# Performance work log

Hardware: AMD Instinct MI355X
Metric: run time of the kernel (lower is better)

## Reference

```python
import jax, jax.numpy as jnp
import numpy as np

NEG_ATT = 0.2   # GATv2Conv internal leaky_relu slope
NEG_ACT = 0.01  # nn.LeakyReLU default slope (activation between layers)

def _segment_softmax(logits, seg, n):
    m = jax.ops.segment_max(logits, seg, num_segments=n)
    ex = jnp.exp(logits - m[seg])
    s = jax.ops.segment_sum(ex, seg, num_segments=n)
    return ex / s[seg]

def _gatv2(h, Wl, bl, Wr, br, att, bias, src, dst, n):
    # PyG GATv2Conv, heads=1: xl = lin_l(h) (source/message), xr = lin_r(h) (target)
    xl = h @ Wl + bl                                   # [N, H]
    xr = h @ Wr + br                                   # [N, H]
    e = jax.nn.leaky_relu(xl[src] + xr[dst], NEG_ATT)  # [E, H]
    logits = e @ att                                   # [E]
    alpha = _segment_softmax(logits, dst, n)           # softmax over incoming edges per dst
    out = jax.ops.segment_sum(xl[src] * alpha[:, None], dst, num_segments=n)
    return out + bias

def setup_inputs() -> dict:
    key = jax.random.key(0)
    G, P, DEG, DIN, H, EX, OUT, NC = 4096, 24, 8, 32, 128, 8, 3, 6
    N = G * P
    E = N * DEG
    ks = jax.random.split(key, 16)
    x = jax.random.normal(ks[0], (N, DIN), jnp.float32)
    gid = jnp.arange(E) // (P * DEG)  # edges stay within their graph
    src = gid * P + jax.random.randint(ks[1], (E,), 0, P)
    dst = gid * P + jax.random.randint(ks[2], (E,), 0, P)
    batch = jnp.repeat(jnp.arange(G), P)
    extra_feat = jax.random.normal(ks[3], (G, EX), jnp.float32)
    sc = lambda k, shp: jax.random.normal(k, shp, jnp.float32) * 0.05
    return dict(
        x=x, src=src, dst=dst, batch=batch, extra_feat=extra_feat,
        W_init0=sc(ks[4], (DIN, H)), b_init0=jnp.zeros((H,), jnp.float32),
        W_init1=sc(ks[5], (H, H)), b_init1=jnp.zeros((H,), jnp.float32),
        Wl=sc(ks[6], (NC, H, H)), bl=jnp.zeros((NC, H), jnp.float32),
        Wr=sc(ks[7], (NC, H, H)), br=jnp.zeros((NC, H), jnp.float32),
        att=sc(ks[8], (NC, H)), cbias=jnp.zeros((NC, H), jnp.float32),
        Wf0=sc(ks[9], (H + EX, H)), bf0=jnp.zeros((H,), jnp.float32),
        Wf1=sc(ks[10], (H, H)), bf1=jnp.zeros((H,), jnp.float32),
        Wf2=sc(ks[11], (H, OUT)), bf2=jnp.zeros((OUT,), jnp.float32),
    )

def reference(x, src, dst, batch, extra_feat,
              W_init0, b_init0, W_init1, b_init1,
              Wl, bl, Wr, br, att, cbias,
              Wf0, bf0, Wf1, bf1, Wf2, bf2):
    N = x.shape[0]
    G = extra_feat.shape[0]
    # init MLP
    h = jax.nn.leaky_relu(x @ W_init0 + b_init0, NEG_ACT)
    h = jax.nn.leaky_relu(h @ W_init1 + b_init1, NEG_ACT)
    # GATv2Conv adds self-loops
    loop = jnp.arange(N)
    src_sl = jnp.concatenate([src, loop])
    dst_sl = jnp.concatenate([dst, loop])
    NUM_GAT, MP = 2, 3
    for g in range(NUM_GAT):
        for m in range(MP):
            c = g * MP + m
            h = _gatv2(h, Wl[c], bl[c], Wr[c], br[c], att[c], cbias[c], src_sl, dst_sl, N)
            if m < MP - 1:  # BasicGNN: act between convs, not after last
                h = jax.nn.leaky_relu(h, NEG_ACT)
    # global_add_pool + extra features + final MLP
    pooled = jax.ops.segment_sum(h, batch, num_segments=G)
    z = jnp.concatenate([pooled, extra_feat], axis=1)
    z = jax.nn.leaky_relu(z @ Wf0 + bf0, NEG_ACT)
    z = jax.nn.leaky_relu(z @ Wf1 + bf1, NEG_ACT)
    return z @ Wf2 + bf2
```

## Files before the change

### kernel.cpp

```cpp
#include <hip/hip_runtime.h>

#define NG   4096
#define P    24
#define EPG  192
#define ESL  216
#define DIN  32
#define H    128
#define EX   8
#define NOUT 3
#define HSS  136
#define XTS  36

typedef _Float16 f16x8 __attribute__((ext_vector_type(8)));
typedef _Float16 h2    __attribute__((ext_vector_type(2)));
typedef float    f32x4 __attribute__((ext_vector_type(4)));

__device__ __forceinline__ unsigned short f2h(float v) {
    _Float16 h = (_Float16)v; unsigned short u; __builtin_memcpy(&u, &h, 2); return u;
}
__device__ __forceinline__ float h2f(unsigned short u) {
    _Float16 h; __builtin_memcpy(&h, &u, 2); return (float)h;
}
__device__ __forceinline__ unsigned pkadd(unsigned a, unsigned b) {
    h2 x, y; __builtin_memcpy(&x, &a, 4); __builtin_memcpy(&y, &b, 4);
    h2 z = x + y; unsigned r; __builtin_memcpy(&r, &z, 4); return r;
}
__device__ __forceinline__ float lrelu(float v, float s) { return v > 0.f ? v : v * s; }

__global__ void cvtw(const float* __restrict__ W0, const float* __restrict__ W1,
                     const float* __restrict__ Wl, const float* __restrict__ Wr,
                     const float* __restrict__ att, const float* __restrict__ bl,
                     const float* __restrict__ br, unsigned short* __restrict__ ws) {
    int i = blockIdx.x * 256 + threadIdx.x;
    if (i < 217088) {
        float v;
        if (i < 4096)        { int n = i >> 5, k = i & 31;  v = W0[k * 128 + n]; }
        else if (i < 20480)  { int j = i - 4096;  int n = j >> 7, k = j & 127; v = W1[k * 128 + n]; }
        else if (i < 118784) { int j = i - 20480; int c = j >> 14, r = j & 16383;
                               int n = r >> 7, k = r & 127; v = Wl[c * 16384 + k * 128 + n]; }
        else                 { int j = i - 118784; int c = j >> 14, r = j & 16383;
                               int n = r >> 7, k = r & 127; v = Wr[c * 16384 + k * 128 + n]; }
        ws[i] = f2h(v);
    } else if (i < 241664) {
        int j = i - 217088;
        const float* W = (j < 12288) ? Wl : Wr;
        if (j >= 12288) j -= 12288;
        int c = j >> 11, r = j & 2047, row = r >> 7, k = r & 127;
        float v = 0.f;
        if (row == 0) {
            for (int q = 0; q < 128; ++q) v += W[c * 16384 + k * 128 + q] * att[c * 128 + q];
        }
        ws[i] = f2h(v);
    } else if (i < 241676) {
        int c = i - 241664;
        const float* B = (c < 6) ? bl : br;
        int cc = (c < 6) ? c : c - 6;
        float s = 0.f;
        for (int q = 0; q < 128; ++q) s += B[cc * 128 + q] * att[cc * 128 + q];
        ((float*)(ws + 241664))[c] = s;
    }
}

__global__ __launch_bounds__(256, 4) void gat_all(
    const float* __restrict__ x,
    const int*   __restrict__ src,
    const int*   __restrict__ dst,
    const float* __restrict__ extra,
    const float* __restrict__ b0,  const float* __restrict__ b1,
    const float* __restrict__ bl,  const float* __restrict__ br,
    const float* __restrict__ att, const float* __restrict__ cbias,
    const float* __restrict__ Wf0, const float* __restrict__ bf0,
    const float* __restrict__ Wf1, const float* __restrict__ bf1,
    const float* __restrict__ Wf2, const float* __restrict__ bf2,
    const unsigned short* __restrict__ wsb,
    float* __restrict__ out)
{
    __shared__ __align__(16) unsigned short hb [32 * HSS];
    __shared__ __align__(16) unsigned short xlb[32 * HSS];
    __shared__ __align__(16) unsigned short xrb[32 * HSS];
    __shared__ __align__(16) unsigned short xlT[128 * XTS];
    __shared__ __align__(16) float          Am[1024];
    __shared__ __align__(16) unsigned int   att_h[64];
    __shared__ float dsum[32];
    __shared__ float snode[64];

    const int g    = blockIdx.x;
    const int t    = threadIdx.x;
    const int lane = t & 63;
    const int w    = t >> 6;
    const int m16  = lane & 15;
    const int kc   = lane >> 4;
    const long long gn = (long long)g * P;

    const unsigned short* W0T = wsb;
    const unsigned short* W1T = wsb + 4096;
    const unsigned short* WLT = wsb + 20480;
    const unsigned short* WRT = wsb + 118784;
    const float* wsf = (const float*)(wsb + 241664);

    int s_e = 0, d_e = 0;
    if (t < ESL) {
        if (t < EPG) {
            s_e = src[(long long)g * EPG + t] - (int)gn;
            d_e = dst[(long long)g * EPG + t] - (int)gn;
        } else { s_e = d_e = t - EPG; }
    }

    if (t < 192) {
        float4 v = *reinterpret_cast<const float4*>(&x[gn * DIN + t * 4]);
        int n = t >> 3, k = (t & 7) * 4;
        *reinterpret_cast<ushort4*>(&xlT[n * XTS + k]) =
            make_ushort4(f2h(v.x), f2h(v.y), f2h(v.z), f2h(v.w));
    } else {
        int u = t - 192;
        int r = 24 + (u >> 3), k = (u & 7) * 4;
        *reinterpret_cast<ushort4*>(&xlT[r * XTS + k]) = make_ushort4(0, 0, 0, 0);
    }
    __syncthreads();

    {
        f32x4 acc[4] = {};
        f16x8 a = *reinterpret_cast<const f16x8*>(&xlT[((w & 1) * 16 + m16) * XTS + kc * 8]);
        #pragma unroll
        for (int i = 0; i < 4; ++i) {
            int nt = (w >> 1) * 4 + i;
            f16x8 b = *reinterpret_cast<const f16x8*>(&W0T[(nt * 16 + m16) * 32 + kc * 8]);
            acc[i] = __builtin_amdgcn_mfma_f32_16x16x32_f16(a, b, acc[i], 0, 0, 0);
        }
        #pragma unroll
        for (int i = 0; i < 4; ++i) {
            int col = (w >> 1) * 64 + i * 16 + m16;
            float bv = b0[col];
            #pragma unroll
            for (int r = 0; r < 4; ++r) {
                int row = (w & 1) * 16 + kc * 4 + r;
                xlb[row * HSS + col] = f2h(lrelu(acc[i][r] + bv, 0.01f));
            }
        }
    }
    __syncthreads();

    {
        f32x4 acc[4] = {};
        for (int kt = 0; kt < 4; ++kt) {
            f16x8 a = *reinterpret_cast<const f16x8*>(&xlb[((w & 1) * 16 + m16) * HSS + kt * 32 + kc * 8]);
            #pragma unroll
            for (int i = 0; i < 4; ++i) {
                int nt = (w >> 1) * 4 + i;
                f16x8 b = *reinterpret_cast<const f16x8*>(&W1T[(nt * 16 + m16) * 128 + kt * 32 + kc * 8]);
                acc[i] = __builtin_amdgcn_mfma_f32_16x16x32_f16(a, b, acc[i], 0, 0, 0);
            }
        }
        #pragma unroll
        for (int i = 0; i < 4; ++i) {
            int col = (w >> 1) * 64 + i * 16 + m16;
            float bv = b1[col];
            #pragma unroll
            for (int r = 0; r < 4; ++r) {
                int row = (w & 1) * 16 + kc * 4 + r;
                hb[row * HSS + col] = f2h(lrelu(acc[i][r] + bv, 0.01f));
            }
        }
    }
    __syncthreads();

    for (int c = 0; c < 6; ++c) {
        *reinterpret_cast<float4*>(&Am[t * 4]) = make_float4(0.f, 0.f, 0.f, 0.f);
        if (t < 32) dsum[t] = (t < P) ? 0.f : 1.0f;
        if (t < 64) att_h[t] = ((unsigned)f2h(att[c * H + 2 * t])) |
                               (((unsigned)f2h(att[c * H + 2 * t + 1])) << 16);

        const unsigned short* WT   = ((w & 1) ? WRT : WLT) + c * 16384;
        const unsigned short* WAX  = wsb + 217088 + ((w & 1) ? 12288 : 0) + c * 2048;
        const float*          bias = ((w & 1) ? br : bl) + c * H;
        f32x4 acc[8] = {};
        f32x4 acce[2] = {};
        for (int kt = 0; kt < 4; ++kt) {
            f16x8 a0 = *reinterpret_cast<const f16x8*>(&hb[(m16)      * HSS + kt * 32 + kc * 8]);
            f16x8 a1 = *reinterpret_cast<const f16x8*>(&hb[(16 + m16) * HSS + kt * 32 + kc * 8]);
            #pragma unroll
            for (int i = 0; i < 4; ++i) {
                int nt = (w >> 1) * 4 + i;
                f16x8 b = *reinterpret_cast<const f16x8*>(&WT[(nt * 16 + m16) * 128 + kt * 32 + kc * 8]);
                acc[i]     = __builtin_amdgcn_mfma_f32_16x16x32_f16(a0, b, acc[i],     0, 0, 0);
                acc[4 + i] = __builtin_amdgcn_mfma_f32_16x16x32_f16(a1, b, acc[4 + i], 0, 0, 0);
            }
            if (w >= 2) {
                f16x8 bx = *reinterpret_cast<const f16x8*>(&WAX[m16 * 128 + kt * 32 + kc * 8]);
                acce[0] = __builtin_amdgcn_mfma_f32_16x16x32_f16(a0, bx, acce[0], 0, 0, 0);
                acce[1] = __builtin_amdgcn_mfma_f32_16x16x32_f16(a1, bx, acce[1], 0, 0, 0);
            }
        }
        {
            unsigned short* XO = (w & 1) ? xrb : xlb;
            const bool isL = !(w & 1);
            #pragma unroll
            for (int mt = 0; mt < 2; ++mt)
            #pragma unroll
            for (int i = 0; i < 4; ++i) {
                int col = (w >> 1) * 64 + i * 16 + m16;
                float bv = bias[col];
                unsigned short ub[4];
                #pragma unroll
                for (int r = 0; r < 4; ++r) {
                    int row = mt * 16 + kc * 4 + r;
                    ub[r] = f2h(acc[mt * 4 + i][r] + bv);
                    XO[row * HSS + col] = ub[r];
                }
                if (isL)
                    *reinterpret_cast<ushort4*>(&xlT[col * XTS + mt * 16 + kc * 4]) =
                        make_ushort4(ub[0], ub[1], ub[2], ub[3]);
            }
            if (w >= 2 && m16 == 0) {
                float cst = (w == 2) ? wsf[c] : wsf[6 + c];
                float* dp = (w == 2) ? snode : (snode + 32);
                #pragma unroll
                for (int mt = 0; mt < 2; ++mt)
                #pragma unroll
                for (int r = 0; r < 4; ++r)
                    dp[mt * 16 + kc * 4 + r] = acce[mt][r] + cst;
            }
        }
        __syncthreads();

        if (t < ESL) {
            const uint4* xa = reinterpret_cast<const uint4*>(&xlb[s_e * HSS]);
            const uint4* xb = reinterpret_cast<const uint4*>(&xrb[d_e * HSS]);
            const uint4* ap = reinterpret_cast<const uint4*>(att_h);
            float a0 = 0.f, a1 = 0.f, a2 = 0.f, a3 = 0.f;
            #pragma unroll 4
            for (int cc = 0; cc < 16; ++cc) {
                uint4 wa = xa[cc], wb = xb[cc], pp = ap[cc];
                unsigned u0 = pkadd(wa.x, wb.x) & 0x7fff7fffu;
                unsigned u1 = pkadd(wa.y, wb.y) & 0x7fff7fffu;
                unsigned u2 = pkadd(wa.z, wb.z) & 0x7fff7fffu;
                unsigned u3 = pkadd(wa.w, wb.w) & 0x7fff7fffu;
                asm volatile("v_dot2_f32_f16 %0, %1, %2, %0" : "+v"(a0) : "v"(u0), "v"(pp.x));
                asm volatile("v_dot2_f32_f16 %0, %1, %2, %0" : "+v"(a1) : "v"(u1), "v"(pp.y));
                asm volatile("v_dot2_f32_f16 %0, %1, %2, %0" : "+v"(a2) : "v"(u2), "v"(pp.z));
                asm volatile("v_dot2_f32_f16 %0, %1, %2, %0" : "+v"(a3) : "v"(u3), "v"(pp.w));
            }
            float abss = (a0 + a1) + (a2 + a3);
            float lg = fmaf(0.6f, snode[s_e] + snode[32 + d_e], 0.4f * abss);
            float ex = __expf(lg);
            atomicAdd(&Am[d_e * 32 + s_e], ex);
            atomicAdd(&dsum[d_e], ex);
        }
        __syncthreads();

        {
            int arow = (w & 1) * 16 + m16;
            float4 u0 = *reinterpret_cast<const float4*>(&Am[arow * 32 + kc * 8]);
            float4 u1 = *reinterpret_cast<const float4*>(&Am[arow * 32 + kc * 8 + 4]);
            f16x8 a;
            a[0] = (_Float16)u0.x; a[1] = (_Float16)u0.y;
            a[2] = (_Float16)u0.z; a[3] = (_Float16)u0.w;
            a[4] = (_Float16)u1.x; a[5] = (_Float16)u1.y;
            a[6] = (_Float16)u1.z; a[7] = (_Float16)u1.w;
            f32x4 acc2[4] = {};
            #pragma unroll
            for (int i = 0; i < 4; ++i) {
                int nt = (w >> 1) * 4 + i;
                f16x8 b = *reinterpret_cast<const f16x8*>(&xlT[(nt * 16 + m16) * XTS + kc * 8]);
                acc2[i] = __builtin_amdgcn_mfma_f32_16x16x32_f16(a, b, acc2[i], 0, 0, 0);
            }
            float inv[4];
            #pragma unroll
            for (int r = 0; r < 4; ++r)
                inv[r] = __builtin_amdgcn_rcpf(dsum[(w & 1) * 16 + kc * 4 + r]);
            const bool doact = (c % 3) < 2;
            #pragma unroll
            for (int i = 0; i < 4; ++i) {
                int col = (w >> 1) * 64 + i * 16 + m16;
                float cb = cbias[c * H + col];
                #pragma unroll
                for (int r = 0; r < 4; ++r) {
                    int row = (w & 1) * 16 + kc * 4 + r;
                    float v = fmaf(acc2[i][r], inv[r], cb);
                    if (doact) v = lrelu(v, 0.01f);
                    hb[row * HSS + col] = f2h(v);
                }
            }
        }
        __syncthreads();
    }

    float* z  = Am;
    float* pa = Am + 144;
    float* pb = Am + 288;
    float* h1 = Am + 432;
    float* qa = Am + 576;
    float* qb = Am + 720;
    float* h2 = Am + 864;
    if (t < H) {
        float s = 0.f;
        for (int r = 0; r < P; ++r) s += h2f(hb[r * HSS + t]);
        z[t] = s;
    } else if (t < H + EX) {
        z[t] = extra[(long long)g * EX + (t - H)];
    }
    __syncthreads();
    {
        int j = t & 127, half = t >> 7;
        float a = half ? 0.f : bf0[j];
        int k0 = half ? 68 : 0, k1 = half ? 136 : 68;
        for (int k = k0; k < k1; ++k) a += z[k] * Wf0[k * H + j];
        (half ? pb : pa)[j] = a;
    }
    __syncthreads();
    if (t < H) h1[t] = lrelu(pa[t] + pb[t], 0.01f);
    __syncthreads();
    {
        int j = t & 127, half = t >> 7;
        float a = half ? 0.f : bf1[j];
        int k0 = half * 64, k1 = k0 + 64;
        for (int k = k0; k < k1; ++k) a += h1[k] * Wf1[k * H + j];
        (half ? qb : qa)[j] = a;
    }
    __syncthreads();
    if (t < H) h2[t] = lrelu(qa[t] + qb[t], 0.01f);
    __syncthreads();
    if (t < NOUT) {
        float a = bf2[t];
        for (int k = 0; k < H; ++k) a += h2[k] * Wf2[k * NOUT + t];
        out[(long long)g * NOUT + t] = a;
    }
}

extern "C" void kernel_launch(void* const* d_in, const int* in_sizes, int n_in,
                              void* d_out, int out_size, void* d_ws, size_t ws_size,
                              hipStream_t stream) {
    (void)in_sizes; (void)n_in; (void)out_size; (void)ws_size;
    const float* x     = (const float*)d_in[0];
    const int*   src   = (const int*)  d_in[1];
    const int*   dst   = (const int*)  d_in[2];
    const float* extra = (const float*)d_in[4];
    const float* W0    = (const float*)d_in[5];
    const float* b0    = (const float*)d_in[6];
    const float* W1    = (const float*)d_in[7];
    const float* b1    = (const float*)d_in[8];
    const float* Wl    = (const float*)d_in[9];
    const float* bl    = (const float*)d_in[10];
    const float* Wr    = (const float*)d_in[11];
    const float* br    = (const float*)d_in[12];
    const float* att   = (const float*)d_in[13];
    const float* cbias = (const float*)d_in[14];
    const float* Wf0   = (const float*)d_in[15];
    const float* bf0   = (const float*)d_in[16];
    const float* Wf1   = (const float*)d_in[17];
    const float* bf1   = (const float*)d_in[18];
    const float* Wf2   = (const float*)d_in[19];
    const float* bf2   = (const float*)d_in[20];
    unsigned short* wsb = (unsigned short*)d_ws;
    float* out = (float*)d_out;

    cvtw<<<945, 256, 0, stream>>>(W0, W1, Wl, Wr, att, bl, br, wsb);
    gat_all<<<NG, 256, 0, stream>>>(x, src, dst, extra, b0, b1, bl, br, att, cbias,
                                    Wf0, bf0, Wf1, bf1, Wf2, bf2, wsb, out);
}
```

Measured before the change: 369.9 us.

## Rewrite GAT kernel as single-wavefront blocks with CSR edge aggregation

Each graph is now handled by one 64-lane wavefront instead of four, so all __syncthreads barriers go away and LDS shrinks to one packed buffer. The attention logits are computed exactly with a packed fp16 leaky-relu, replacing the abs-based split that needed precomputed att-projected weights; those weights are dropped from the weight-conversion kernel. Aggregation now walks a per-destination CSR edge list built with LDS atomics, replacing the dense 32x32 attention matrix multiplied by MFMA. Output stores are packed in pairs via DPP, and the final MLP runs with one wave and shuffle reductions. The trade-off is less parallelism per graph, with each wave doing all the MFMA work serially, relying on more resident blocks to hide latency.

```diff
diff --git a/kernel.cpp b/kernel.cpp
--- a/kernel.cpp
+++ b/kernel.cpp
@@ -3,13 +3,21 @@
 #define NG   4096
 #define P    24
 #define EPG  192
-#define ESL  216
 #define DIN  32
 #define H    128
-#define EX   8
 #define NOUT 3
 #define HSS  136
-#define XTS  36
+#define XSS  40
+
+#define O_HB    0
+#define O_XLB   6528
+#define O_XRB   13056
+#define O_ALP   19584
+#define O_DSUM  20448
+#define O_ELIST 20576
+#define O_EOFF  21008
+#define O_ATH   21072
+#define LDS_SZ  21376
 
 typedef _Float16 f16x8 __attribute__((ext_vector_type(8)));
 typedef _Float16 h2    __attribute__((ext_vector_type(2)));
@@ -25,7 +33,22 @@
     h2 x, y; __builtin_memcpy(&x, &a, 4); __builtin_memcpy(&y, &b, 4);
     h2 z = x + y; unsigned r; __builtin_memcpy(&r, &z, 4); return r;
 }
+__device__ __forceinline__ unsigned lrpk(unsigned u) {
+    h2 x; __builtin_memcpy(&x, &u, 4);
+    h2 y = x * (h2){(_Float16)0.2f, (_Float16)0.2f};
+    h2 m; m[0] = x[0] > y[0] ? x[0] : y[0]; m[1] = x[1] > y[1] ? x[1] : y[1];
+    unsigned r; __builtin_memcpy(&r, &m, 4); return r;
+}
 __device__ __forceinline__ float lrelu(float v, float s) { return v > 0.f ? v : v * s; }
+
+#define STPAIR(BASE, ROW, COL, VAL)                                           \
+    do {                                                                      \
+        unsigned o_ = (unsigned)__builtin_amdgcn_mov_dpp(                     \
+            (int)(unsigned)(VAL), 0xB1, 0xF, 0xF, true);                      \
+        if (!(lane & 1))                                                      \
+            *reinterpret_cast<unsigned*>(&(BASE)[(ROW) * HSS + (COL)]) =      \
+                (unsigned)(VAL) | (o_ << 16);                                 \
+    } while (0)
 
 __global__ void cvtw(const float* __restrict__ W0, const float* __restrict__ W1,
                      const float* __restrict__ Wl, const float* __restrict__ Wr,
@@ -41,27 +64,10 @@
         else                 { int j = i - 118784; int c = j >> 14, r = j & 16383;
                                int n = r >> 7, k = r & 127; v = Wr[c * 16384 + k * 128 + n]; }
         ws[i] = f2h(v);
-    } else if (i < 241664) {
-        int j = i - 217088;
-        const float* W = (j < 12288) ? Wl : Wr;
-        if (j >= 12288) j -= 12288;
-        int c = j >> 11, r = j & 2047, row = r >> 7, k = r & 127;
-        float v = 0.f;
-        if (row == 0) {
-            for (int q = 0; q < 128; ++q) v += W[c * 16384 + k * 128 + q] * att[c * 128 + q];
-        }
-        ws[i] = f2h(v);
-    } else if (i < 241676) {
-        int c = i - 241664;
-        const float* B = (c < 6) ? bl : br;
-        int cc = (c < 6) ? c : c - 6;
-        float s = 0.f;
-        for (int q = 0; q < 128; ++q) s += B[cc * 128 + q] * att[cc * 128 + q];
-        ((float*)(ws + 241664))[c] = s;
-    }
-}
-
-__global__ __launch_bounds__(256, 4) void gat_all(
+    }
+}
+
+__global__ __launch_bounds__(64, 2) void gat_all(
     const float* __restrict__ x,
     const int*   __restrict__ src,
     const int*   __restrict__ dst,
@@ -75,19 +81,19 @@
     const unsigned short* __restrict__ wsb,
     float* __restrict__ out)
 {
-    __shared__ __align__(16) unsigned short hb [32 * HSS];
-    __shared__ __align__(16) unsigned short xlb[32 * HSS];
-    __shared__ __align__(16) unsigned short xrb[32 * HSS];
-    __shared__ __align__(16) unsigned short xlT[128 * XTS];
-    __shared__ __align__(16) float          Am[1024];
-    __shared__ __align__(16) unsigned int   att_h[64];
-    __shared__ float dsum[32];
-    __shared__ float snode[64];
+    __shared__ __align__(16) unsigned char L[LDS_SZ];
+    unsigned short* hb    = (unsigned short*)(L + O_HB);
+    unsigned short* xlb   = (unsigned short*)(L + O_XLB);
+    unsigned short* xrb   = (unsigned short*)(L + O_XRB);
+    float*          alp   = (float*)(L + O_ALP);
+    float*          dsF   = (float*)(L + O_DSUM);
+    int*            dsI   = (int*)(L + O_DSUM);
+    unsigned short* elist = (unsigned short*)(L + O_ELIST);
+    unsigned short* eoff  = (unsigned short*)(L + O_EOFF);
+    unsigned*       ath   = (unsigned*)(L + O_ATH);
 
     const int g    = blockIdx.x;
-    const int t    = threadIdx.x;
-    const int lane = t & 63;
-    const int w    = t >> 6;
+    const int lane = threadIdx.x;
     const int m16  = lane & 15;
     const int kc   = lane >> 4;
     const long long gn = (long long)g * P;
@@ -96,234 +102,264 @@
     const unsigned short* W1T = wsb + 4096;
     const unsigned short* WLT = wsb + 20480;
     const unsigned short* WRT = wsb + 118784;
-    const float* wsf = (const float*)(wsb + 241664);
-
-    int s_e = 0, d_e = 0;
-    if (t < ESL) {
-        if (t < EPG) {
-            s_e = src[(long long)g * EPG + t] - (int)gn;
-            d_e = dst[(long long)g * EPG + t] - (int)gn;
-        } else { s_e = d_e = t - EPG; }
-    }
-
-    if (t < 192) {
-        float4 v = *reinterpret_cast<const float4*>(&x[gn * DIN + t * 4]);
-        int n = t >> 3, k = (t & 7) * 4;
-        *reinterpret_cast<ushort4*>(&xlT[n * XTS + k]) =
-            make_ushort4(f2h(v.x), f2h(v.y), f2h(v.z), f2h(v.w));
-    } else {
-        int u = t - 192;
-        int r = 24 + (u >> 3), k = (u & 7) * 4;
-        *reinterpret_cast<ushort4*>(&xlT[r * XTS + k]) = make_ushort4(0, 0, 0, 0);
-    }
-    __syncthreads();
-
-    {
-        f32x4 acc[4] = {};
-        f16x8 a = *reinterpret_cast<const f16x8*>(&xlT[((w & 1) * 16 + m16) * XTS + kc * 8]);
-        #pragma unroll
-        for (int i = 0; i < 4; ++i) {
-            int nt = (w >> 1) * 4 + i;
+
+    int es[4], ed[4];
+    #pragma unroll
+    for (int q = 0; q < 3; ++q) {
+        es[q] = src[(long long)g * EPG + lane + 64 * q] - (int)gn;
+        ed[q] = dst[(long long)g * EPG + lane + 64 * q] - (int)gn;
+    }
+    es[3] = ed[3] = lane;
+    const int ne = (lane < P) ? 4 : 3;
+
+    {
+        unsigned short* XS = hb;
+        #pragma unroll
+        for (int i = 0; i < 12; ++i) {
+            int idx = lane + i * 64;
+            XS[(idx >> 5) * XSS + (idx & 31)] = f2h(x[gn * DIN + idx]);
+        }
+        #pragma unroll
+        for (int i = 0; i < 5; ++i) XS[960 + lane + i * 64] = 0;
+    }
+
+    if (lane < 32) dsI[lane] = 0;
+    #pragma unroll
+    for (int q = 0; q < 4; ++q) if (q < ne) atomicAdd(&dsI[ed[q]], 1);
+    {
+        int v = (lane < P) ? dsI[lane] : 0;
+        #pragma unroll
+        for (int dlt = 1; dlt <= 16; dlt <<= 1) {
+            int u = __shfl_up(v, dlt);
+            if (lane >= dlt) v += u;
+        }
+        if (lane < P) eoff[lane + 1] = (unsigned short)v;
+        if (lane == 0) eoff[0] = 0;
+    }
+    if (lane < 32) dsI[lane] = 0;
+    #pragma unroll
+    for (int q = 0; q < 4; ++q) if (q < ne) {
+        int pos = atomicAdd(&dsI[ed[q]], 1);
+        int eid = (q < 3) ? (lane + 64 * q) : (192 + lane);
+        elist[eoff[ed[q]] + pos] = (unsigned short)((es[q] << 8) | eid);
+    }
+
+    {
+        unsigned short* XS = hb;
+        f16x8 a0 = *reinterpret_cast<const f16x8*>(&XS[(m16)      * XSS + kc * 8]);
+        f16x8 a1 = *reinterpret_cast<const f16x8*>(&XS[(16 + m16) * XSS + kc * 8]);
+        #pragma unroll
+        for (int nt = 0; nt < 8; ++nt) {
+            f32x4 c0 = {}, c1 = {};
             f16x8 b = *reinterpret_cast<const f16x8*>(&W0T[(nt * 16 + m16) * 32 + kc * 8]);
-            acc[i] = __builtin_amdgcn_mfma_f32_16x16x32_f16(a, b, acc[i], 0, 0, 0);
-        }
-        #pragma unroll
-        for (int i = 0; i < 4; ++i) {
-            int col = (w >> 1) * 64 + i * 16 + m16;
+            c0 = __builtin_amdgcn_mfma_f32_16x16x32_f16(a0, b, c0, 0, 0, 0);
+            c1 = __builtin_amdgcn_mfma_f32_16x16x32_f16(a1, b, c1, 0, 0, 0);
+            int col = nt * 16 + m16;
             float bv = b0[col];
             #pragma unroll
             for (int r = 0; r < 4; ++r) {
-                int row = (w & 1) * 16 + kc * 4 + r;
-                xlb[row * HSS + col] = f2h(lrelu(acc[i][r] + bv, 0.01f));
-            }
-        }
-    }
-    __syncthreads();
-
-    {
-        f32x4 acc[4] = {};
-        for (int kt = 0; kt < 4; ++kt) {
-            f16x8 a = *reinterpret_cast<const f16x8*>(&xlb[((w & 1) * 16 + m16) * HSS + kt * 32 + kc * 8]);
+                unsigned short ub = f2h(lrelu(c0[r] + bv, 0.01f));
+                STPAIR(xlb, kc * 4 + r, col, ub);
+            }
+            if (kc < 2) {
+                #pragma unroll
+                for (int r = 0; r < 4; ++r) {
+                    unsigned short ub = f2h(lrelu(c1[r] + bv, 0.01f));
+                    STPAIR(xlb, 16 + kc * 4 + r, col, ub);
+                }
+            }
+        }
+    }
+
+    {
+        f16x8 a[2][4];
+        #pragma unroll
+        for (int mt = 0; mt < 2; ++mt)
+        #pragma unroll
+        for (int kt = 0; kt < 4; ++kt)
+            a[mt][kt] = *reinterpret_cast<const f16x8*>(&xlb[(mt * 16 + m16) * HSS + kt * 32 + kc * 8]);
+        #pragma unroll
+        for (int nt = 0; nt < 8; ++nt) {
+            f32x4 c0 = {}, c1 = {};
             #pragma unroll
-            for (int i = 0; i < 4; ++i) {
-                int nt = (w >> 1) * 4 + i;
+            for (int kt = 0; kt < 4; ++kt) {
                 f16x8 b = *reinterpret_cast<const f16x8*>(&W1T[(nt * 16 + m16) * 128 + kt * 32 + kc * 8]);
-                acc[i] = __builtin_amdgcn_mfma_f32_16x16x32_f16(a, b, acc[i], 0, 0, 0);
-            }
-        }
-        #pragma unroll
-        for (int i = 0; i < 4; ++i) {
-            int col = (w >> 1) * 64 + i * 16 + m16;
+                c0 = __builtin_amdgcn_mfma_f32_16x16x32_f16(a[0][kt], b, c0, 0, 0, 0);
+                c1 = __builtin_amdgcn_mfma_f32_16x16x32_f16(a[1][kt], b, c1, 0, 0, 0);
+            }
+            int col = nt * 16 + m16;
             float bv = b1[col];
             #pragma unroll
             for (int r = 0; r < 4; ++r) {
-                int row = (w & 1) * 16 + kc * 4 + r;
-                hb[row * HSS + col] = f2h(lrelu(acc[i][r] + bv, 0.01f));
-            }
-        }
-    }
-    __syncthreads();
-
-    for (int c = 0; c < 6; ++c) {
-        *reinterpret_cast<float4*>(&Am[t * 4]) = make_float4(0.f, 0.f, 0.f, 0.f);
-        if (t < 32) dsum[t] = (t < P) ? 0.f : 1.0f;
-        if (t < 64) att_h[t] = ((unsigned)f2h(att[c * H + 2 * t])) |
-                               (((unsigned)f2h(att[c * H + 2 * t + 1])) << 16);
-
-        const unsigned short* WT   = ((w & 1) ? WRT : WLT) + c * 16384;
-        const unsigned short* WAX  = wsb + 217088 + ((w & 1) ? 12288 : 0) + c * 2048;
-        const float*          bias = ((w & 1) ? br : bl) + c * H;
-        f32x4 acc[8] = {};
-        f32x4 acce[2] = {};
-        for (int kt = 0; kt < 4; ++kt) {
-            f16x8 a0 = *reinterpret_cast<const f16x8*>(&hb[(m16)      * HSS + kt * 32 + kc * 8]);
-            f16x8 a1 = *reinterpret_cast<const f16x8*>(&hb[(16 + m16) * HSS + kt * 32 + kc * 8]);
-            #pragma unroll
-            for (int i = 0; i < 4; ++i) {
-                int nt = (w >> 1) * 4 + i;
-                f16x8 b = *reinterpret_cast<const f16x8*>(&WT[(nt * 16 + m16) * 128 + kt * 32 + kc * 8]);
-                acc[i]     = __builtin_amdgcn_mfma_f32_16x16x32_f16(a0, b, acc[i],     0, 0, 0);
-                acc[4 + i] = __builtin_amdgcn_mfma_f32_16x16x32_f16(a1, b, acc[4 + i], 0, 0, 0);
-            }
-            if (w >= 2) {
-                f16x8 bx = *reinterpret_cast<const f16x8*>(&WAX[m16 * 128 + kt * 32 + kc * 8]);
-                acce[0] = __builtin_amdgcn_mfma_f32_16x16x32_f16(a0, bx, acce[0], 0, 0, 0);
-                acce[1] = __builtin_amdgcn_mfma_f32_16x16x32_f16(a1, bx, acce[1], 0, 0, 0);
-            }
-        }
-        {
-            unsigned short* XO = (w & 1) ? xrb : xlb;
-            const bool isL = !(w & 1);
-            #pragma unroll
-            for (int mt = 0; mt < 2; ++mt)
-            #pragma unroll
-            for (int i = 0; i < 4; ++i) {
-                int col = (w >> 1) * 64 + i * 16 + m16;
-                float bv = bias[col];
-                unsigned short ub[4];
+                unsigned short ub = f2h(lrelu(c0[r] + bv, 0.01f));
+                STPAIR(hb, kc * 4 + r, col, ub);
+            }
+            if (kc < 2) {
                 #pragma unroll
                 for (int r = 0; r < 4; ++r) {
-                    int row = mt * 16 + kc * 4 + r;
-                    ub[r] = f2h(acc[mt * 4 + i][r] + bv);
-                    XO[row * HSS + col] = ub[r];
-                }
-                if (isL)
-                    *reinterpret_cast<ushort4*>(&xlT[col * XTS + mt * 16 + kc * 4]) =
-                        make_ushort4(ub[0], ub[1], ub[2], ub[3]);
-            }
-            if (w >= 2 && m16 == 0) {
-                float cst = (w == 2) ? wsf[c] : wsf[6 + c];
-                float* dp = (w == 2) ? snode : (snode + 32);
+                    unsigned short ub = f2h(lrelu(c1[r] + bv, 0.01f));
+                    STPAIR(hb, 16 + kc * 4 + r, col, ub);
+                }
+            }
+        }
+    }
+
+    for (int c = 0; c < 6; ++c) {
+        f16x8 a[2][4];
+        #pragma unroll
+        for (int mt = 0; mt < 2; ++mt)
+        #pragma unroll
+        for (int kt = 0; kt < 4; ++kt)
+            a[mt][kt] = *reinterpret_cast<const f16x8*>(&hb[(mt * 16 + m16) * HSS + kt * 32 + kc * 8]);
+        #pragma unroll
+        for (int mm = 0; mm < 2; ++mm) {
+            const unsigned short* WT = (mm ? WRT : WLT) + c * 16384;
+            const float* bias = (mm ? br : bl) + c * H;
+            unsigned short* XO = mm ? xrb : xlb;
+            #pragma unroll
+            for (int nt = 0; nt < 8; ++nt) {
+                f32x4 c0 = {}, c1 = {};
                 #pragma unroll
-                for (int mt = 0; mt < 2; ++mt)
+                for (int kt = 0; kt < 4; ++kt) {
+                    f16x8 b = *reinterpret_cast<const f16x8*>(&WT[(nt * 16 + m16) * 128 + kt * 32 + kc * 8]);
+                    c0 = __builtin_amdgcn_mfma_f32_16x16x32_f16(a[0][kt], b, c0, 0, 0, 0);
+                    c1 = __builtin_amdgcn_mfma_f32_16x16x32_f16(a[1][kt], b, c1, 0, 0, 0);
+                }
+                int col = nt * 16 + m16;
+                float bv = bias[col];
                 #pragma unroll
-                for (int r = 0; r < 4; ++r)
-                    dp[mt * 16 + kc * 4 + r] = acce[mt][r] + cst;
-            }
-        }
-        __syncthreads();
-
-        if (t < ESL) {
-            const uint4* xa = reinterpret_cast<const uint4*>(&xlb[s_e * HSS]);
-            const uint4* xb = reinterpret_cast<const uint4*>(&xrb[d_e * HSS]);
-            const uint4* ap = reinterpret_cast<const uint4*>(att_h);
-            float a0 = 0.f, a1 = 0.f, a2 = 0.f, a3 = 0.f;
+                for (int r = 0; r < 4; ++r) {
+                    unsigned short ub = f2h(c0[r] + bv);
+                    STPAIR(XO, kc * 4 + r, col, ub);
+                }
+                if (kc < 2) {
+                    #pragma unroll
+                    for (int r = 0; r < 4; ++r) {
+                        unsigned short ub = f2h(c1[r] + bv);
+                        STPAIR(XO, 16 + kc * 4 + r, col, ub);
+                    }
+                }
+            }
+        }
+
+        if (lane < 32) dsF[lane] = 0.f;
+        ath[lane] = (unsigned)f2h(att[c * H + 2 * lane]) |
+                    ((unsigned)f2h(att[c * H + 2 * lane + 1]) << 16);
+        #pragma unroll
+        for (int q = 0; q < 4; ++q) if (q < ne) {
+            const int s = es[q], d = ed[q];
+            const uint4* xa = reinterpret_cast<const uint4*>(&xlb[s * HSS]);
+            const uint4* xb = reinterpret_cast<const uint4*>(&xrb[d * HSS]);
+            const uint4* ap = reinterpret_cast<const uint4*>(ath);
+            float t0 = 0.f, t1 = 0.f, t2 = 0.f, t3 = 0.f;
             #pragma unroll 4
             for (int cc = 0; cc < 16; ++cc) {
                 uint4 wa = xa[cc], wb = xb[cc], pp = ap[cc];
-                unsigned u0 = pkadd(wa.x, wb.x) & 0x7fff7fffu;
-                unsigned u1 = pkadd(wa.y, wb.y) & 0x7fff7fffu;
-                unsigned u2 = pkadd(wa.z, wb.z) & 0x7fff7fffu;
-                unsigned u3 = pkadd(wa.w, wb.w) & 0x7fff7fffu;
-                asm volatile("v_dot2_f32_f16 %0, %1, %2, %0" : "+v"(a0) : "v"(u0), "v"(pp.x));
-                asm volatile("v_dot2_f32_f16 %0, %1, %2, %0" : "+v"(a1) : "v"(u1), "v"(pp.y));
-                asm volatile("v_dot2_f32_f16 %0, %1, %2, %0" : "+v"(a2) : "v"(u2), "v"(pp.z));
-                asm volatile("v_dot2_f32_f16 %0, %1, %2, %0" : "+v"(a3) : "v"(u3), "v"(pp.w));
-            }
-            float abss = (a0 + a1) + (a2 + a3);
-            float lg = fmaf(0.6f, snode[s_e] + snode[32 + d_e], 0.4f * abss);
-            float ex = __expf(lg);
-            atomicAdd(&Am[d_e * 32 + s_e], ex);
-            atomicAdd(&dsum[d_e], ex);
-        }
-        __syncthreads();
+                unsigned u0 = lrpk(pkadd(wa.x, wb.x));
+                unsigned u1 = lrpk(pkadd(wa.y, wb.y));
+                unsigned u2 = lrpk(pkadd(wa.z, wb.z));
+                unsigned u3 = lrpk(pkadd(wa.w, wb.w));
+                asm volatile("v_dot2_f32_f16 %0, %1, %2, %0" : "+v"(t0) : "v"(u0), "v"(pp.x));
+                asm volatile("v_dot2_f32_f16 %0, %1, %2, %0" : "+v"(t1) : "v"(u1), "v"(pp.y));
+                asm volatile("v_dot2_f32_f16 %0, %1, %2, %0" : "+v"(t2) : "v"(u2), "v"(pp.z));
+                asm volatile("v_dot2_f32_f16 %0, %1, %2, %0" : "+v"(t3) : "v"(u3), "v"(pp.w));
+            }
+            float ex = __expf((t0 + t1) + (t2 + t3));
+            int eid = (q < 3) ? (lane + 64 * q) : (192 + lane);
+            alp[eid] = ex;
+            atomicAdd(&dsF[d], ex);
+        }
 
         {
-            int arow = (w & 1) * 16 + m16;
-            float4 u0 = *reinterpret_cast<const float4*>(&Am[arow * 32 + kc * 8]);
-            float4 u1 = *reinterpret_cast<const float4*>(&Am[arow * 32 + kc * 8 + 4]);
-            f16x8 a;
-            a[0] = (_Float16)u0.x; a[1] = (_Float16)u0.y;
-            a[2] = (_Float16)u0.z; a[3] = (_Float16)u0.w;
-            a[4] = (_Float16)u1.x; a[5] = (_Float16)u1.y;
-            a[6] = (_Float16)u1.z; a[7] = (_Float16)u1.w;
-            f32x4 acc2[4] = {};
-            #pragma unroll
-            for (int i = 0; i < 4; ++i) {
-                int nt = (w >> 1) * 4 + i;
-                f16x8 b = *reinterpret_cast<const f16x8*>(&xlT[(nt * 16 + m16) * XTS + kc * 8]);
-                acc2[i] = __builtin_amdgcn_mfma_f32_16x16x32_f16(a, b, acc2[i], 0, 0, 0);
-            }
-            float inv[4];
-            #pragma unroll
-            for (int r = 0; r < 4; ++r)
-                inv[r] = __builtin_amdgcn_rcpf(dsum[(w & 1) * 16 + kc * 4 + r]);
+            const int half = lane >> 5, c4 = (lane & 31) * 4;
             const bool doact = (c % 3) < 2;
-            #pragma unroll
-            for (int i = 0; i < 4; ++i) {
-                int col = (w >> 1) * 64 + i * 16 + m16;
-                float cb = cbias[c * H + col];
-                #pragma unroll
-                for (int r = 0; r < 4; ++r) {
-                    int row = (w & 1) * 16 + kc * 4 + r;
-                    float v = fmaf(acc2[i][r], inv[r], cb);
-                    if (doact) v = lrelu(v, 0.01f);
-                    hb[row * HSS + col] = f2h(v);
-                }
-            }
-        }
-        __syncthreads();
-    }
-
-    float* z  = Am;
-    float* pa = Am + 144;
-    float* pb = Am + 288;
-    float* h1 = Am + 432;
-    float* qa = Am + 576;
-    float* qb = Am + 720;
-    float* h2 = Am + 864;
-    if (t < H) {
-        float s = 0.f;
-        for (int r = 0; r < P; ++r) s += h2f(hb[r * HSS + t]);
-        z[t] = s;
-    } else if (t < H + EX) {
-        z[t] = extra[(long long)g * EX + (t - H)];
-    }
-    __syncthreads();
-    {
-        int j = t & 127, half = t >> 7;
-        float a = half ? 0.f : bf0[j];
-        int k0 = half ? 68 : 0, k1 = half ? 136 : 68;
-        for (int k = k0; k < k1; ++k) a += z[k] * Wf0[k * H + j];
-        (half ? pb : pa)[j] = a;
-    }
-    __syncthreads();
-    if (t < H) h1[t] = lrelu(pa[t] + pb[t], 0.01f);
-    __syncthreads();
-    {
-        int j = t & 127, half = t >> 7;
-        float a = half ? 0.f : bf1[j];
-        int k0 = half * 64, k1 = k0 + 64;
-        for (int k = k0; k < k1; ++k) a += h1[k] * Wf1[k * H + j];
-        (half ? qb : qa)[j] = a;
-    }
-    __syncthreads();
-    if (t < H) h2[t] = lrelu(qa[t] + qb[t], 0.01f);
-    __syncthreads();
-    if (t < NOUT) {
-        float a = bf2[t];
-        for (int k = 0; k < H; ++k) a += h2[k] * Wf2[k * NOUT + t];
-        out[(long long)g * NOUT + t] = a;
+            float4 cb4 = *reinterpret_cast<const float4*>(&cbias[c * H + c4]);
+            #pragma unroll 2
+            for (int np = 0; np < 12; ++np) {
+                int n = np * 2 + half;
+                int q1 = eoff[n + 1];
+                float s0 = 0.f, s1 = 0.f, s2 = 0.f, s3 = 0.f;
+                for (int q = eoff[n]; q < q1; ++q) {
+                    unsigned e = elist[q];
+                    float al = alp[e & 255];
+                    uint2 wv = *reinterpret_cast<const uint2*>(&xlb[(e >> 8) * HSS + c4]);
+                    s0 = fmaf(h2f((unsigned short)wv.x), al, s0);
+                    s1 = fmaf(h2f((unsigned short)(wv.x >> 16)), al, s1);
+                    s2 = fmaf(h2f((unsigned short)wv.y), al, s2);
+                    s3 = fmaf(h2f((unsigned short)(wv.y >> 16)), al, s3);
+                }
+                float inv = __builtin_amdgcn_rcpf(dsF[n]);
+                float o0 = fmaf(s0, inv, cb4.x);
+                float o1 = fmaf(s1, inv, cb4.y);
+                float o2 = fmaf(s2, inv, cb4.z);
+                float o3 = fmaf(s3, inv, cb4.w);
+                if (doact) {
+                    o0 = lrelu(o0, 0.01f); o1 = lrelu(o1, 0.01f);
+                    o2 = lrelu(o2, 0.01f); o3 = lrelu(o3, 0.01f);
+                }
+                uint2 pk;
+                pk.x = (unsigned)f2h(o0) | ((unsigned)f2h(o1) << 16);
+                pk.y = (unsigned)f2h(o2) | ((unsigned)f2h(o3) << 16);
+                *reinterpret_cast<uint2*>(&hb[n * HSS + c4]) = pk;
+            }
+        }
+    }
+
+    float* z = alp;
+    {
+        float p0 = 0.f, p1 = 0.f;
+        #pragma unroll
+        for (int r = 0; r < P; ++r) {
+            unsigned wv = *reinterpret_cast<const unsigned*>(&hb[r * HSS + lane * 2]);
+            p0 += h2f((unsigned short)wv);
+            p1 += h2f((unsigned short)(wv >> 16));
+        }
+        z[lane * 2] = p0; z[lane * 2 + 1] = p1;
+        if (lane < 8) z[128 + lane] = extra[(long long)g * 8 + lane];
+    }
+    float* h1 = (float*)(L + O_ALP + 576);
+    {
+        int j0 = lane * 2;
+        float a0 = bf0[j0], a1 = bf0[j0 + 1];
+        for (int k = 0; k < H + 8; ++k) {
+            float zk = z[k];
+            float2 wv = *reinterpret_cast<const float2*>(&Wf0[k * H + j0]);
+            a0 = fmaf(zk, wv.x, a0); a1 = fmaf(zk, wv.y, a1);
+        }
+        h1[j0] = lrelu(a0, 0.01f); h1[j0 + 1] = lrelu(a1, 0.01f);
+    }
+    float* hv2 = z;
+    {
+        int j0 = lane * 2;
+        float a0 = bf1[j0], a1 = bf1[j0 + 1];
+        for (int k = 0; k < H; ++k) {
+            float hk = h1[k];
+            float2 wv = *reinterpret_cast<const float2*>(&Wf1[k * H + j0]);
+            a0 = fmaf(hk, wv.x, a0); a1 = fmaf(hk, wv.y, a1);
+        }
+        hv2[j0] = lrelu(a0, 0.01f); hv2[j0 + 1] = lrelu(a1, 0.01f);
+    }
+    {
+        float p0 = 0.f, p1 = 0.f, p2 = 0.f;
+        #pragma unroll
+        for (int kk = 0; kk < 2; ++kk) {
+            int k = lane * 2 + kk;
+            float hk = hv2[k];
+            p0 = fmaf(hk, Wf2[k * NOUT + 0], p0);
+            p1 = fmaf(hk, Wf2[k * NOUT + 1], p1);
+            p2 = fmaf(hk, Wf2[k * NOUT + 2], p2);
+        }
+        #pragma unroll
+        for (int d = 1; d < 64; d <<= 1) {
+            p0 += __shfl_xor(p0, d);
+            p1 += __shfl_xor(p1, d);
+            p2 += __shfl_xor(p2, d);
+        }
+        if (lane == 0) {
+            out[(long long)g * NOUT + 0] = p0 + bf2[0];
+            out[(long long)g * NOUT + 1] = p1 + bf2[1];
+            out[(long long)g * NOUT + 2] = p2 + bf2[2];
+        }
     }
 }
 
@@ -354,7 +390,7 @@
     unsigned short* wsb = (unsigned short*)d_ws;
     float* out = (float*)d_out;
 
-    cvtw<<<945, 256, 0, stream>>>(W0, W1, Wl, Wr, att, bl, br, wsb);
-    gat_all<<<NG, 256, 0, stream>>>(x, src, dst, extra, b0, b1, bl, br, att, cbias,
-                                    Wf0, bf0, Wf1, bf1, Wf2, bf2, wsb, out);
-}
+    cvtw<<<848, 256, 0, stream>>>(W0, W1, Wl, Wr, att, bl, br, wsb);
+    gat_all<<<NG, 64, 0, stream>>>(x, src, dst, extra, b0, b1, bl, br, att, cbias,
+                                   Wf0, bf0, Wf1, bf1, Wf2, bf2, wsb, out);
+}
```

Measured after the change: 632.7 us. 71.1% more time.
